# Performance work log

Measured on AMD Instinct MI355X. Metric: run time of the kernel, lower is better.

Reference implementation:

```python
import jax, jax.numpy as jnp
import numpy as np
import math

D_MODEL = 1024
N_HEADS = 16
D_K = D_MODEL // N_HEADS
THRESH = 0.1  # attention probs below this are zeroed


def setup_inputs() -> dict:
    key = jax.random.key(0)
    ks = jax.random.split(key, 9)
    B, S, D = 2, 2048, D_MODEL
    scale = 1.0 / math.sqrt(D)
    x = jax.random.normal(ks[0], (B, S, D), dtype=jnp.float32)
    Wq = jax.random.normal(ks[1], (D, D), dtype=jnp.float32) * scale
    bq = jax.random.normal(ks[2], (D,), dtype=jnp.float32) * 0.01
    Wk = jax.random.normal(ks[3], (D, D), dtype=jnp.float32) * scale
    bk = jax.random.normal(ks[4], (D,), dtype=jnp.float32) * 0.01
    Wv = jax.random.normal(ks[5], (D, D), dtype=jnp.float32) * scale
    bv = jax.random.normal(ks[6], (D,), dtype=jnp.float32) * 0.01
    Wo = jax.random.normal(ks[7], (D, D), dtype=jnp.float32) * scale
    bo = jax.random.normal(ks[8], (D,), dtype=jnp.float32) * 0.01
    return {"x": x, "Wq": Wq, "bq": bq, "Wk": Wk, "bk": bk,
            "Wv": Wv, "bv": bv, "Wo": Wo, "bo": bo}


def _split_heads(t):
    B, S, D = t.shape
    return t.reshape(B, S, N_HEADS, D_K).transpose(0, 2, 1, 3)  # [B,H,S,dk]


def reference(x, Wq, bq, Wk, bk, Wv, bv, Wo, bo):
    # torch nn.Linear: y = x @ W.T + b
    q = _split_heads(x @ Wq.T + bq)
    k = _split_heads(x @ Wk.T + bk)
    v = _split_heads(x @ Wv.T + bv)
    scores = jnp.einsum('bhqd,bhkd->bhqk', q, k) / math.sqrt(D_K)
    probs = jax.nn.softmax(scores, axis=-1)          # full unmasked softmax (returned)
    keep = probs >= THRESH                            # ~low_attention_mask
    probs_model = jnp.where(keep, probs, 0.0)        # masked_fill; dropout is identity in eval
    ctx = jnp.einsum('bhqk,bhkd->bhqd', probs_model, v)
    B, H, S, dk = ctx.shape
    merged = ctx.transpose(0, 2, 1, 3).reshape(B, S, H * dk)
    out = merged @ Wo.T + bo
    attention_sum = probs.sum(axis=1)                # [B,S,S] sum over heads
    attention_mask = keep.astype(jnp.float32).sum(axis=1)  # [B,S,S]
    return (out, attention_sum, attention_mask)
```

## Files before the change

### kernel.cpp

```cpp
#include <hip/hip_runtime.h>

#define SDIM 2048
#define DDIM 1024
#define NH 16
#define DK 64
#define NB 2
#define MROWS (NB * SDIM)
#define MAXEV 65536
#define EXPC 0.18033688011112f
#define L01 -3.3219281f

typedef _Float16 f16x8 __attribute__((ext_vector_type(8)));
typedef _Float16 f16x4 __attribute__((ext_vector_type(4)));
typedef float f32x4 __attribute__((ext_vector_type(4)));

__device__ __forceinline__ void ld_lds16(const _Float16* g, _Float16* l) {
  __builtin_amdgcn_global_load_lds(
      (const __attribute__((address_space(1))) void*)g,
      (__attribute__((address_space(3))) void*)l, 16, 0, 0);
}

__global__ __launch_bounds__(256) void cvt_f16(
    const float* __restrict__ x, const float* __restrict__ wq,
    const float* __restrict__ wk, const float* __restrict__ wv,
    _Float16* __restrict__ xh, _Float16* __restrict__ wqh,
    _Float16* __restrict__ wkh, _Float16* __restrict__ wvh) {
  int i = blockIdx.x * 256 + threadIdx.x;
  const float* src;
  _Float16* dst;
  int off;
  if (i < 1048576) {
    src = x; dst = xh; off = i;
  } else if (i < 1310720) {
    src = wq; dst = wqh; off = i - 1048576;
  } else if (i < 1572864) {
    src = wk; dst = wkh; off = i - 1310720;
  } else {
    src = wv; dst = wvh; off = i - 1572864;
  }
  float4 v = ((const float4*)src)[off];
  f16x4 h;
  h[0] = (_Float16)v.x; h[1] = (_Float16)v.y;
  h[2] = (_Float16)v.z; h[3] = (_Float16)v.w;
  ((f16x4*)dst)[off] = h;
}

__global__ __launch_bounds__(256, 2) void proj_gemm(
    const _Float16* __restrict__ xh, const _Float16* __restrict__ Wqh,
    const _Float16* __restrict__ Wkh, const _Float16* __restrict__ Wvh,
    const float* __restrict__ bq, const float* __restrict__ bk,
    const float* __restrict__ bv, _Float16* __restrict__ Qo,
    _Float16* __restrict__ Ko, float* __restrict__ Vo) {
  __shared__ _Float16 sA[128 * 64];
  __shared__ _Float16 sB[128 * 64];
  const int t = threadIdx.x;
  const int lane = t & 63, wv = t >> 6;
  const int lr = lane & 15, quad = lane >> 4;
  const int wm = wv >> 1, wn = wv & 1;
  const int m0 = blockIdx.y * 128, n0 = blockIdx.x * 128;
  const int z = blockIdx.z;
  const _Float16* Bp = z == 0 ? Wqh : (z == 1 ? Wkh : Wvh);
  const float* bias = z == 0 ? bq : (z == 1 ? bk : bv);

  const int strow = t >> 3;
  const int stchunk = t & 7;
  const int stsrc = (stchunk ^ (strow & 7)) * 8;

  f32x4 acc[4][4];
#pragma unroll
  for (int i = 0; i < 4; ++i)
#pragma unroll
    for (int j = 0; j < 4; ++j) acc[i][j] = (f32x4){0.f, 0.f, 0.f, 0.f};

  for (int k0 = 0; k0 < DDIM; k0 += 64) {
    __syncthreads();
#pragma unroll
    for (int i = 0; i < 4; ++i) {
      const int row = i * 32 + strow;
      ld_lds16(&xh[(size_t)(m0 + row) * DDIM + k0 + stsrc],
               &sA[row * 64 + stchunk * 8]);
      ld_lds16(&Bp[(size_t)(n0 + row) * DDIM + k0 + stsrc],
               &sB[row * 64 + stchunk * 8]);
    }
    __syncthreads();
    f16x8 af[4][2], bf[4][2];
#pragma unroll
    for (int i = 0; i < 4; ++i)
#pragma unroll
      for (int kk = 0; kk < 2; ++kk) {
        const int ph = ((kk * 4 + quad) ^ (lr & 7)) * 8;
        af[i][kk] = *(const f16x8*)&sA[(wm * 64 + i * 16 + lr) * 64 + ph];
        bf[i][kk] = *(const f16x8*)&sB[(wn * 64 + i * 16 + lr) * 64 + ph];
      }
#pragma unroll
    for (int kk = 0; kk < 2; ++kk)
#pragma unroll
      for (int i = 0; i < 4; ++i)
#pragma unroll
        for (int j = 0; j < 4; ++j)
          acc[i][j] = __builtin_amdgcn_mfma_f32_16x16x32_f16(
              af[i][kk], bf[j][kk], acc[i][j], 0, 0, 0);
  }
#pragma unroll
  for (int j = 0; j < 4; ++j) {
    const int ng = n0 + wn * 64 + j * 16 + lr;
    const float bvv = bias[ng];
    const int h = ng >> 6, d = ng & 63;
#pragma unroll
    for (int i = 0; i < 4; ++i) {
#pragma unroll
      for (int r = 0; r < 4; ++r) {
        const int mg = m0 + wm * 64 + i * 16 + quad * 4 + r;
        const int b = mg >> 11, s = mg & 2047;
        const float o = acc[i][j][r] + bvv;
        const size_t off = ((size_t)(b * NH + h) * SDIM + s) * DK + d;
        if (z == 0)
          Qo[off] = (_Float16)(o * EXPC);
        else if (z == 1)
          Ko[off] = (_Float16)o;
        else
          Vo[off] = o;
      }
    }
  }
}

__global__ __launch_bounds__(256) void attn_denom(const _Float16* __restrict__ Q,
                                                  const _Float16* __restrict__ K,
                                                  float* __restrict__ laOut) {
  __shared__ _Float16 Ks[128 * 64];
  const int t = threadIdx.x;
  const int lane = t & 63, wave = t >> 6;
  const int quad = lane >> 4, lr = lane & 15;
  const int q0 = blockIdx.x * 64;
  const int bh = blockIdx.y;
  const _Float16* Qh = Q + (size_t)bh * SDIM * DK;
  const _Float16* Kh = K + (size_t)bh * SDIM * DK;
  const size_t qoff = (size_t)(q0 + wave * 16 + lr) * DK + quad * 8;
  const f16x8 aq0 = *(const f16x8*)&Qh[qoff];
  const f16x8 aq1 = *(const f16x8*)&Qh[qoff + 32];
  const int strow = t >> 3, stchunk = t & 7;
  const int stsrc = (stchunk ^ (strow & 7)) * 8;
  const int ph0 = (quad ^ (lr & 7)) * 8;
  const int ph1 = ((4 + quad) ^ (lr & 7)) * 8;

  float dsum[4] = {0.f, 0.f, 0.f, 0.f};
#pragma unroll 1
  for (int kt = 0; kt < 16; ++kt) {
    __syncthreads();
#pragma unroll
    for (int i = 0; i < 4; ++i)
      ld_lds16(&Kh[(size_t)(kt * 128 + i * 32 + strow) * DK + stsrc],
               &Ks[(i * 32 + strow) * 64 + stchunk * 8]);
    __syncthreads();
#pragma unroll
    for (int c = 0; c < 8; ++c) {
      f16x8 b0 = *(const f16x8*)&Ks[(c * 16 + lr) * 64 + ph0];
      f16x8 b1 = *(const f16x8*)&Ks[(c * 16 + lr) * 64 + ph1];
      f32x4 acc = {0.f, 0.f, 0.f, 0.f};
      acc = __builtin_amdgcn_mfma_f32_16x16x32_f16(aq0, b0, acc, 0, 0, 0);
      acc = __builtin_amdgcn_mfma_f32_16x16x32_f16(aq1, b1, acc, 0, 0, 0);
#pragma unroll
      for (int r = 0; r < 4; ++r)
        dsum[r] += __builtin_amdgcn_exp2f(acc[r]);
    }
  }
#pragma unroll
  for (int m = 1; m < 16; m <<= 1)
#pragma unroll
    for (int r = 0; r < 4; ++r)
      dsum[r] += __shfl_xor(dsum[r], m, 64);
  if (lr == 0) {
#pragma unroll
    for (int r = 0; r < 4; ++r)
      laOut[(size_t)bh * SDIM + q0 + wave * 16 + quad * 4 + r] =
          -__builtin_amdgcn_logf(dsum[r]);
  }
}

__global__ __launch_bounds__(256) void attn_pass2(
    const _Float16* __restrict__ Q, const _Float16* __restrict__ K,
    const float* __restrict__ la, float* __restrict__ attSum,
    float* __restrict__ attMask, float4* __restrict__ ev,
    int* __restrict__ ecnt) {
  __shared__ float SMEM[64 * 68];
  _Float16* Khs = (_Float16*)SMEM;
  float* Tbuf = SMEM;
  const int t = threadIdx.x;
  const int lane = t & 63, wave = t >> 6;
  const int quad = lane >> 4, lr = lane & 15;
  const int k0 = blockIdx.x * 64;
  const int q0 = blockIdx.y * 64;
  const int b = blockIdx.z;
  const int strow = t >> 3, stchunk = t & 7;
  const int stsrc = (stchunk ^ (strow & 7)) * 8;
  const int ph0 = (quad ^ (lr & 7)) * 8;
  const int ph1 = ((4 + quad) ^ (lr & 7)) * 8;

  const size_t qbase = ((size_t)(b * NH) * SDIM + q0 + wave * 16 + lr) * DK;
  const size_t dbase = (size_t)(b * NH) * SDIM + q0 + wave * 16 + quad * 4;
  const size_t hstep = (size_t)SDIM * DK;

  float asum[4][4] = {};
  float amask[4][4] = {};
  float mx = -1e30f;

#pragma unroll 1
  for (int hp = 0; hp < 8; ++hp) {
    __syncthreads();
#pragma unroll
    for (int hh = 0; hh < 2; ++hh) {
      const _Float16* Kp =
          K + (size_t)(b * NH + 2 * hp + hh) * hstep + (size_t)k0 * DK;
#pragma unroll
      for (int i = 0; i < 2; ++i)
        ld_lds16(&Kp[(size_t)(i * 32 + strow) * DK + stsrc],
                 &Khs[hh * 4096 + (i * 32 + strow) * 64 + stchunk * 8]);
    }
    f16x8 a0[2], a1[2];
    float4 lav[2];
#pragma unroll
    for (int hh = 0; hh < 2; ++hh) {
      const size_t ho = (size_t)(2 * hp + hh) * hstep;
      a0[hh] = *(const f16x8*)&Q[qbase + ho + quad * 8];
      a1[hh] = *(const f16x8*)&Q[qbase + ho + 32 + quad * 8];
      lav[hh] = *(const float4*)&la[dbase + (size_t)(2 * hp + hh) * SDIM];
    }
    __syncthreads();
#pragma unroll
    for (int hh = 0; hh < 2; ++hh) {
      const _Float16* Ks = &Khs[hh * 4096];
      const float lar[4] = {lav[hh].x, lav[hh].y, lav[hh].z, lav[hh].w};
#pragma unroll
      for (int c = 0; c < 4; ++c) {
        f16x8 b0 = *(const f16x8*)&Ks[(c * 16 + lr) * 64 + ph0];
        f16x8 b1 = *(const f16x8*)&Ks[(c * 16 + lr) * 64 + ph1];
        f32x4 acc = {0.f, 0.f, 0.f, 0.f};
        acc = __builtin_amdgcn_mfma_f32_16x16x32_f16(a0[hh], b0, acc, 0, 0, 0);
        acc = __builtin_amdgcn_mfma_f32_16x16x32_f16(a1[hh], b1, acc, 0, 0, 0);
#pragma unroll
        for (int r = 0; r < 4; ++r) {
          const float arg = acc[r] + lar[r];
          mx = fmaxf(mx, arg);
          asum[c][r] += __builtin_amdgcn_exp2f(arg);
        }
      }
    }
  }
  if (__any(mx >= L01)) {
#pragma unroll 1
    for (int h = 0; h < NH; ++h) {
      const _Float16* Kp =
          K + (size_t)(b * NH + h) * hstep + (size_t)k0 * DK;
      const size_t ho = (size_t)h * hstep;
      const f16x8 aq0 = *(const f16x8*)&Q[qbase + ho + quad * 8];
      const f16x8 aq1 = *(const f16x8*)&Q[qbase + ho + 32 + quad * 8];
      const float4 l4 = *(const float4*)&la[dbase + (size_t)h * SDIM];
      const float lar[4] = {l4.x, l4.y, l4.z, l4.w};
#pragma unroll 1
      for (int c = 0; c < 4; ++c) {
        const f16x8 b0 = *(const f16x8*)&Kp[(c * 16 + lr) * DK + quad * 8];
        const f16x8 b1 = *(const f16x8*)&Kp[(c * 16 + lr) * DK + 32 + quad * 8];
        f32x4 acc = {0.f, 0.f, 0.f, 0.f};
        acc = __builtin_amdgcn_mfma_f32_16x16x32_f16(aq0, b0, acc, 0, 0, 0);
        acc = __builtin_amdgcn_mfma_f32_16x16x32_f16(aq1, b1, acc, 0, 0, 0);
#pragma unroll 1
        for (int r = 0; r < 4; ++r) {
          const float p = __builtin_amdgcn_exp2f(acc[r] + lar[r]);
          if (p >= 0.1f) {
            amask[c][r] += 1.0f;
            int idx = atomicAdd(ecnt, 1);
            if (idx < MAXEV)
              ev[idx] = make_float4(
                  __int_as_float(b * NH + h),
                  __int_as_float(q0 + wave * 16 + quad * 4 + r),
                  __int_as_float(k0 + c * 16 + lr), p);
          }
        }
      }
    }
  }
  const int orow = t >> 2, ocol = (t & 3) * 16;
  __syncthreads();
#pragma unroll
  for (int c = 0; c < 4; ++c)
#pragma unroll
    for (int r = 0; r < 4; ++r)
      Tbuf[(wave * 16 + quad * 4 + r) * 68 + c * 16 + lr] = asum[c][r];
  __syncthreads();
#pragma unroll
  for (int j = 0; j < 4; ++j) {
    float4 v = *(float4*)&Tbuf[orow * 68 + ocol + j * 4];
    *(float4*)&attSum[((size_t)(b * SDIM) + q0 + orow) * SDIM + k0 + ocol +
                      j * 4] = v;
  }
  __syncthreads();
#pragma unroll
  for (int c = 0; c < 4; ++c)
#pragma unroll
    for (int r = 0; r < 4; ++r)
      Tbuf[(wave * 16 + quad * 4 + r) * 68 + c * 16 + lr] = amask[c][r];
  __syncthreads();
#pragma unroll
  for (int j = 0; j < 4; ++j) {
    float4 v = *(float4*)&Tbuf[orow * 68 + ocol + j * 4];
    *(float4*)&attMask[((size_t)(b * SDIM) + q0 + orow) * SDIM + k0 + ocol +
                       j * 4] = v;
  }
}

__global__ __launch_bounds__(64) void apply_events(
    const float4* __restrict__ ev, const int* __restrict__ ecnt,
    const float* __restrict__ V, float* __restrict__ merged,
    int* __restrict__ flags) {
  int n = *ecnt;
  if (n > MAXEV) n = MAXEV;
  const int d = threadIdx.x;
  for (int e = blockIdx.x; e < n; e += gridDim.x) {
    float4 r = ev[e];
    int bh = __float_as_int(r.x);
    int q = __float_as_int(r.y);
    int kc = __float_as_int(r.z);
    float p = r.w;
    int b = bh >> 4, h = bh & 15;
    atomicAdd(&merged[((size_t)(b * SDIM + q)) * DDIM + h * DK + d],
              p * V[((size_t)bh * SDIM + kc) * DK + d]);
    if (d == 0) flags[b * SDIM + q] = 1;
  }
}

__global__ __launch_bounds__(256) void out_gemm(const float* __restrict__ A,
                                                const float* __restrict__ W,
                                                const float* __restrict__ bias,
                                                float* __restrict__ out,
                                                const int* __restrict__ flags) {
  __shared__ float As[16][68];
  __shared__ float Ws[16][68];
  __shared__ int anyF;
  const int t = threadIdx.x;
  const int tx = t & 15, ty = t >> 4;
  const int m0 = blockIdx.y * 64;
  const int n0 = blockIdx.x * 64;
  if (t == 0) anyF = 0;
  __syncthreads();
  if (t < 64 && flags[m0 + t]) anyF = 1;
  __syncthreads();
  const int nb = n0 + tx * 4;
  const float4 bv = *(const float4*)&bias[nb];
  if (!anyF) {
#pragma unroll
    for (int r = 0; r < 4; ++r)
      *(float4*)&out[(size_t)(m0 + ty * 4 + r) * DDIM + nb] = bv;
    return;
  }
  const int lr = t >> 2;
  const int lc = (t & 3) * 4;
  float acc[4][4] = {};
  for (int k0 = 0; k0 < DDIM; k0 += 16) {
    __syncthreads();
    float4 av = *(const float4*)&A[(size_t)(m0 + lr) * DDIM + k0 + lc];
    float4 wv = *(const float4*)&W[(size_t)(n0 + lr) * DDIM + k0 + lc];
    As[lc + 0][lr] = av.x; As[lc + 1][lr] = av.y;
    As[lc + 2][lr] = av.z; As[lc + 3][lr] = av.w;
    Ws[lc + 0][lr] = wv.x; Ws[lc + 1][lr] = wv.y;
    Ws[lc + 2][lr] = wv.z; Ws[lc + 3][lr] = wv.w;
    __syncthreads();
#pragma unroll
    for (int kk = 0; kk < 16; ++kk) {
      float4 a4 = *(const float4*)&As[kk][ty * 4];
      float4 b4 = *(const float4*)&Ws[kk][tx * 4];
      const float a[4] = {a4.x, a4.y, a4.z, a4.w};
      const float b[4] = {b4.x, b4.y, b4.z, b4.w};
#pragma unroll
      for (int r = 0; r < 4; ++r)
#pragma unroll
        for (int c = 0; c < 4; ++c)
          acc[r][c] = fmaf(a[r], b[c], acc[r][c]);
    }
  }
#pragma unroll
  for (int r = 0; r < 4; ++r) {
    float4 o;
    o.x = acc[r][0] + bv.x;
    o.y = acc[r][1] + bv.y;
    o.z = acc[r][2] + bv.z;
    o.w = acc[r][3] + bv.w;
    *(float4*)&out[(size_t)(m0 + ty * 4 + r) * DDIM + nb] = o;
  }
}

extern "C" void kernel_launch(void* const* d_in, const int* in_sizes, int n_in,
                              void* d_out, int out_size, void* d_ws,
                              size_t ws_size, hipStream_t stream) {
  const float* x = (const float*)d_in[0];
  const float* Wq = (const float*)d_in[1];
  const float* bq = (const float*)d_in[2];
  const float* Wk = (const float*)d_in[3];
  const float* bk = (const float*)d_in[4];
  const float* Wv = (const float*)d_in[5];
  const float* bv = (const float*)d_in[6];
  const float* Wo = (const float*)d_in[7];
  const float* bo = (const float*)d_in[8];

  float* out = (float*)d_out;
  float* attSum = out + (size_t)MROWS * DDIM;
  float* attMask = attSum + (size_t)NB * SDIM * SDIM;

  char* ws = (char*)d_ws;
  const size_t bigF = (size_t)MROWS * DDIM * sizeof(float);
  const size_t bigH = (size_t)MROWS * DDIM * sizeof(_Float16);
  const size_t wH = (size_t)DDIM * DDIM * sizeof(_Float16);
  _Float16* Qh = (_Float16*)ws;  ws += bigH;
  _Float16* Kh = (_Float16*)ws;  ws += bigH;
  float* V = (float*)ws;         ws += bigF;
  float* merged = (float*)ws;    ws += bigF;
  _Float16* xh = (_Float16*)ws;  ws += bigH;
  _Float16* Wqh = (_Float16*)ws; ws += wH;
  _Float16* Wkh = (_Float16*)ws; ws += wH;
  _Float16* Wvh = (_Float16*)ws; ws += wH;
  float* laBuf = (float*)ws;     ws += (size_t)NB * NH * SDIM * sizeof(float);
  float4* ev = (float4*)ws;      ws += (size_t)MAXEV * sizeof(float4);
  int* flags = (int*)ws;         ws += (size_t)MROWS * sizeof(int);
  int* ecnt = (int*)ws;          ws += 16;

  hipMemsetAsync(merged, 0, bigF, stream);
  hipMemsetAsync(flags, 0, (size_t)MROWS * sizeof(int), stream);
  hipMemsetAsync(ecnt, 0, 16, stream);

  dim3 blk(256);
  cvt_f16<<<dim3(7168), blk, 0, stream>>>(x, Wq, Wk, Wv, xh, Wqh, Wkh, Wvh);
  proj_gemm<<<dim3(8, 32, 3), blk, 0, stream>>>(xh, Wqh, Wkh, Wvh, bq, bk, bv,
                                                Qh, Kh, V);
  attn_denom<<<dim3(32, 32), blk, 0, stream>>>(Qh, Kh, laBuf);
  attn_pass2<<<dim3(32, 32, 2), blk, 0, stream>>>(Qh, Kh, laBuf, attSum,
                                                  attMask, ev, ecnt);
  apply_events<<<dim3(256), dim3(64), 0, stream>>>(ev, ecnt, V, merged, flags);
  out_gemm<<<dim3(16, 64), blk, 0, stream>>>(merged, Wo, bo, out, flags);
}
```

Baseline: 260.3 us.

## Double-buffer K tiles in attention kernels and store outputs directly with nontemporal writes

```diff
diff --git a/kernel.cpp b/kernel.cpp
--- a/kernel.cpp
+++ b/kernel.cpp
@@ -128,7 +128,8 @@
 __global__ __launch_bounds__(256) void attn_denom(const _Float16* __restrict__ Q,
                                                   const _Float16* __restrict__ K,
                                                   float* __restrict__ laOut) {
-  __shared__ _Float16 Ks[128 * 64];
+  __shared__ _Float16 KdA[128 * 64];
+  __shared__ _Float16 KdB[128 * 64];
   const int t = threadIdx.x;
   const int lane = t & 63, wave = t >> 6;
   const int quad = lane >> 4, lr = lane & 15;
@@ -144,26 +145,34 @@
   const int ph0 = (quad ^ (lr & 7)) * 8;
   const int ph1 = ((4 + quad) ^ (lr & 7)) * 8;
 
+#define STAGE_DN(KT, BUF)                                                  \
+  {                                                                        \
+    _Pragma("unroll") for (int i = 0; i < 4; ++i)                          \
+        ld_lds16(&Kh[(size_t)((KT)*128 + i * 32 + strow) * DK + stsrc],    \
+                 &BUF[(i * 32 + strow) * 64 + stchunk * 8]);               \
+  }
+
+#define COMPUTE_DN(BUF)                                                    \
+  _Pragma("unroll") for (int c = 0; c < 8; ++c) {                          \
+    f16x8 b0 = *(const f16x8*)&BUF[(c * 16 + lr) * 64 + ph0];              \
+    f16x8 b1 = *(const f16x8*)&BUF[(c * 16 + lr) * 64 + ph1];              \
+    f32x4 acc = {0.f, 0.f, 0.f, 0.f};                                      \
+    acc = __builtin_amdgcn_mfma_f32_16x16x32_f16(aq0, b0, acc, 0, 0, 0);   \
+    acc = __builtin_amdgcn_mfma_f32_16x16x32_f16(aq1, b1, acc, 0, 0, 0);   \
+    _Pragma("unroll") for (int r = 0; r < 4; ++r)                          \
+        dsum[r] += __builtin_amdgcn_exp2f(acc[r]);                         \
+  }
+
   float dsum[4] = {0.f, 0.f, 0.f, 0.f};
+  STAGE_DN(0, KdA);
 #pragma unroll 1
-  for (int kt = 0; kt < 16; ++kt) {
-    __syncthreads();
-#pragma unroll
-    for (int i = 0; i < 4; ++i)
-      ld_lds16(&Kh[(size_t)(kt * 128 + i * 32 + strow) * DK + stsrc],
-               &Ks[(i * 32 + strow) * 64 + stchunk * 8]);
-    __syncthreads();
-#pragma unroll
-    for (int c = 0; c < 8; ++c) {
-      f16x8 b0 = *(const f16x8*)&Ks[(c * 16 + lr) * 64 + ph0];
-      f16x8 b1 = *(const f16x8*)&Ks[(c * 16 + lr) * 64 + ph1];
-      f32x4 acc = {0.f, 0.f, 0.f, 0.f};
-      acc = __builtin_amdgcn_mfma_f32_16x16x32_f16(aq0, b0, acc, 0, 0, 0);
-      acc = __builtin_amdgcn_mfma_f32_16x16x32_f16(aq1, b1, acc, 0, 0, 0);
-#pragma unroll
-      for (int r = 0; r < 4; ++r)
-        dsum[r] += __builtin_amdgcn_exp2f(acc[r]);
-    }
+  for (int kt = 0; kt < 16; kt += 2) {
+    __syncthreads();
+    STAGE_DN(kt + 1, KdB);
+    COMPUTE_DN(KdA);
+    __syncthreads();
+    if (kt + 2 < 16) STAGE_DN(kt + 2, KdA);
+    COMPUTE_DN(KdB);
   }
 #pragma unroll
   for (int m = 1; m < 16; m <<= 1)
@@ -176,6 +185,8 @@
       laOut[(size_t)bh * SDIM + q0 + wave * 16 + quad * 4 + r] =
           -__builtin_amdgcn_logf(dsum[r]);
   }
+#undef STAGE_DN
+#undef COMPUTE_DN
 }
 
 __global__ __launch_bounds__(256) void attn_pass2(
@@ -183,9 +194,8 @@
     const float* __restrict__ la, float* __restrict__ attSum,
     float* __restrict__ attMask, float4* __restrict__ ev,
     int* __restrict__ ecnt) {
-  __shared__ float SMEM[64 * 68];
-  _Float16* Khs = (_Float16*)SMEM;
-  float* Tbuf = SMEM;
+  __shared__ _Float16 KbufA[2 * 4096];
+  __shared__ _Float16 KbufB[2 * 4096];
   const int t = threadIdx.x;
   const int lane = t & 63, wave = t >> 6;
   const int quad = lane >> 4, lr = lane & 15;
@@ -205,48 +215,65 @@
   float amask[4][4] = {};
   float mx = -1e30f;
 
+  f16x8 a0[2], a1[2];
+  float4 lav[2];
+
+#define STAGE_P2(HP, BUF)                                                    \
+  {                                                                          \
+    _Pragma("unroll") for (int hh = 0; hh < 2; ++hh) {                       \
+      const _Float16* Kp =                                                   \
+          K + (size_t)(b * NH + 2 * (HP) + hh) * hstep + (size_t)k0 * DK;    \
+      _Pragma("unroll") for (int i = 0; i < 2; ++i)                          \
+          ld_lds16(&Kp[(size_t)(i * 32 + strow) * DK + stsrc],               \
+                   &BUF[hh * 4096 + (i * 32 + strow) * 64 + stchunk * 8]);   \
+    }                                                                        \
+  }
+
+#define LOADQ_P2(HP)                                                         \
+  {                                                                          \
+    _Pragma("unroll") for (int hh = 0; hh < 2; ++hh) {                       \
+      const size_t ho = (size_t)(2 * (HP) + hh) * hstep;                     \
+      a0[hh] = *(const f16x8*)&Q[qbase + ho + quad * 8];                     \
+      a1[hh] = *(const f16x8*)&Q[qbase + ho + 32 + quad * 8];                \
+      lav[hh] = *(const float4*)&la[dbase + (size_t)(2 * (HP) + hh) * SDIM]; \
+    }                                                                        \
+  }
+
+#define COMPUTE_P2(BUF)                                                      \
+  _Pragma("unroll") for (int hh = 0; hh < 2; ++hh) {                         \
+    const _Float16* Ksh = &BUF[hh * 4096];                                   \
+    const float lar[4] = {lav[hh].x, lav[hh].y, lav[hh].z, lav[hh].w};       \
+    _Pragma("unroll") for (int c = 0; c < 4; ++c) {                          \
+      f16x8 b0 = *(const f16x8*)&Ksh[(c * 16 + lr) * 64 + ph0];              \
+      f16x8 b1 = *(const f16x8*)&Ksh[(c * 16 + lr) * 64 + ph1];              \
+      f32x4 acc = {0.f, 0.f, 0.f, 0.f};                                      \
+      acc = __builtin_amdgcn_mfma_f32_16x16x32_f16(a0[hh], b0, acc, 0, 0, 0);\
+      acc = __builtin_amdgcn_mfma_f32_16x16x32_f16(a1[hh], b1, acc, 0, 0, 0);\
+      _Pragma("unroll") for (int r = 0; r < 4; ++r) {                        \
+        const float arg = acc[r] + lar[r];                                   \
+        mx = fmaxf(mx, arg);                                                 \
+        asum[c][r] += __builtin_amdgcn_exp2f(arg);                           \
+      }                                                                      \
+    }                                                                        \
+  }
+
+  STAGE_P2(0, KbufA);
+  LOADQ_P2(0);
 #pragma unroll 1
-  for (int hp = 0; hp < 8; ++hp) {
-    __syncthreads();
-#pragma unroll
-    for (int hh = 0; hh < 2; ++hh) {
-      const _Float16* Kp =
-          K + (size_t)(b * NH + 2 * hp + hh) * hstep + (size_t)k0 * DK;
-#pragma unroll
-      for (int i = 0; i < 2; ++i)
-        ld_lds16(&Kp[(size_t)(i * 32 + strow) * DK + stsrc],
-                 &Khs[hh * 4096 + (i * 32 + strow) * 64 + stchunk * 8]);
-    }
-    f16x8 a0[2], a1[2];
-    float4 lav[2];
-#pragma unroll
-    for (int hh = 0; hh < 2; ++hh) {
-      const size_t ho = (size_t)(2 * hp + hh) * hstep;
-      a0[hh] = *(const f16x8*)&Q[qbase + ho + quad * 8];
-      a1[hh] = *(const f16x8*)&Q[qbase + ho + 32 + quad * 8];
-      lav[hh] = *(const float4*)&la[dbase + (size_t)(2 * hp + hh) * SDIM];
-    }
-    __syncthreads();
-#pragma unroll
-    for (int hh = 0; hh < 2; ++hh) {
-      const _Float16* Ks = &Khs[hh * 4096];
-      const float lar[4] = {lav[hh].x, lav[hh].y, lav[hh].z, lav[hh].w};
-#pragma unroll
-      for (int c = 0; c < 4; ++c) {
-        f16x8 b0 = *(const f16x8*)&Ks[(c * 16 + lr) * 64 + ph0];
-        f16x8 b1 = *(const f16x8*)&Ks[(c * 16 + lr) * 64 + ph1];
-        f32x4 acc = {0.f, 0.f, 0.f, 0.f};
-        acc = __builtin_amdgcn_mfma_f32_16x16x32_f16(a0[hh], b0, acc, 0, 0, 0);
-        acc = __builtin_amdgcn_mfma_f32_16x16x32_f16(a1[hh], b1, acc, 0, 0, 0);
-#pragma unroll
-        for (int r = 0; r < 4; ++r) {
-          const float arg = acc[r] + lar[r];
-          mx = fmaxf(mx, arg);
-          asum[c][r] += __builtin_amdgcn_exp2f(arg);
-        }
-      }
-    }
-  }
+  for (int hp = 0; hp < 8; hp += 2) {
+    __syncthreads();
+    STAGE_P2(hp + 1, KbufB);
+    COMPUTE_P2(KbufA);
+    LOADQ_P2(hp + 1);
+    __syncthreads();
+    if (hp + 2 < 8) STAGE_P2(hp + 2, KbufA);
+    COMPUTE_P2(KbufB);
+    if (hp + 2 < 8) LOADQ_P2(hp + 2);
+  }
+#undef STAGE_P2
+#undef LOADQ_P2
+#undef COMPUTE_P2
+
   if (__any(mx >= L01)) {
 #pragma unroll 1
     for (int h = 0; h < NH; ++h) {
@@ -280,33 +307,15 @@
       }
     }
   }
-  const int orow = t >> 2, ocol = (t & 3) * 16;
-  __syncthreads();
 #pragma unroll
   for (int c = 0; c < 4; ++c)
 #pragma unroll
-    for (int r = 0; r < 4; ++r)
-      Tbuf[(wave * 16 + quad * 4 + r) * 68 + c * 16 + lr] = asum[c][r];
-  __syncthreads();
-#pragma unroll
-  for (int j = 0; j < 4; ++j) {
-    float4 v = *(float4*)&Tbuf[orow * 68 + ocol + j * 4];
-    *(float4*)&attSum[((size_t)(b * SDIM) + q0 + orow) * SDIM + k0 + ocol +
-                      j * 4] = v;
-  }
-  __syncthreads();
-#pragma unroll
-  for (int c = 0; c < 4; ++c)
-#pragma unroll
-    for (int r = 0; r < 4; ++r)
-      Tbuf[(wave * 16 + quad * 4 + r) * 68 + c * 16 + lr] = amask[c][r];
-  __syncthreads();
-#pragma unroll
-  for (int j = 0; j < 4; ++j) {
-    float4 v = *(float4*)&Tbuf[orow * 68 + ocol + j * 4];
-    *(float4*)&attMask[((size_t)(b * SDIM) + q0 + orow) * SDIM + k0 + ocol +
-                       j * 4] = v;
-  }
+    for (int r = 0; r < 4; ++r) {
+      const size_t row = (size_t)(b * SDIM) + q0 + wave * 16 + quad * 4 + r;
+      const size_t col = (size_t)k0 + c * 16 + lr;
+      __builtin_nontemporal_store(asum[c][r], &attSum[row * SDIM + col]);
+      __builtin_nontemporal_store(amask[c][r], &attMask[row * SDIM + col]);
+    }
 }
 
 __global__ __launch_bounds__(64) void apply_events(
```

Measured after the change: 256.3 us. About the same (-1.5%).
